# Performance work log

Hardware: AMD Instinct MI355X
Metric: run time of the kernel (lower is better)

Reference implementation:

```python
import jax, jax.numpy as jnp
import numpy as np

B, C, CI, H, W = 4, 128, 64, 96, 96  # batch, in_channels, inter_channels, spatial
SS = 2                                # sub_sample_factor (maxpool on phi and g)
BN_EPS = 1e-5


def conv1x1(x, w, b):
    # x: [B,C,H,W], w: [O,C], b: [O]
    return jnp.einsum('bchw,oc->bohw', x, w) + b[None, :, None, None]


def maxpool2(x):
    # 2x2 max pool, stride 2. x: [B,C,H,W]
    b, c, h, w = x.shape
    return x.reshape(b, c, h // 2, 2, w // 2, 2).max(axis=(3, 5))


def setup_inputs() -> dict:
    key = jax.random.key(0)
    ks = jax.random.split(key, 12)
    s_in = 1.0 / np.sqrt(C)
    s_ci = 1.0 / np.sqrt(CI)
    return {
        'x':        jax.random.normal(ks[0], (B, C, H, W), jnp.float32),
        'g_w':      jax.random.normal(ks[1], (CI, C), jnp.float32) * s_in,
        'g_b':      jax.random.normal(ks[2], (CI,), jnp.float32) * 0.01,
        'theta_w':  jax.random.normal(ks[3], (CI, C), jnp.float32) * s_in,
        'theta_b':  jax.random.normal(ks[4], (CI,), jnp.float32) * 0.01,
        'phi_w':    jax.random.normal(ks[5], (CI, C), jnp.float32) * s_in,
        'phi_b':    jax.random.normal(ks[6], (CI,), jnp.float32) * 0.01,
        'W_w':      jax.random.normal(ks[7], (C, CI), jnp.float32) * s_ci,
        'W_b':      jax.random.normal(ks[8], (C,), jnp.float32) * 0.01,
        'bn_gamma': jax.random.normal(ks[9], (C,), jnp.float32) * 0.1 + 1.0,
        'bn_beta':  jax.random.normal(ks[10], (C,), jnp.float32) * 0.1,
        'bn_mean':  jax.random.normal(ks[11], (C,), jnp.float32) * 0.1,
        'bn_var':   jax.random.uniform(jax.random.fold_in(key, 99), (C,), jnp.float32, 0.5, 1.5),
    }


def reference(x, g_w, g_b, theta_w, theta_b, phi_w, phi_b, W_w, W_b,
              bn_gamma, bn_beta, bn_mean, bn_var):
    b = x.shape[0]
    # g: conv1x1 -> maxpool(2) -> [B, N_kv, CI]
    g_x = maxpool2(conv1x1(x, g_w, g_b)).reshape(b, CI, -1).transpose(0, 2, 1)
    # theta: conv1x1 -> [B, N_q, CI]
    theta_x = conv1x1(x, theta_w, theta_b).reshape(b, CI, -1).transpose(0, 2, 1)
    # phi: conv1x1 -> maxpool(2) -> [B, CI, N_kv]
    phi_x = maxpool2(conv1x1(x, phi_w, phi_b)).reshape(b, CI, -1)
    # full affinity [B, N_q, N_kv], softmax over keys (embedded_gaussian)
    f = jnp.einsum('bqc,bck->bqk', theta_x, phi_x)
    attn = jax.nn.softmax(f, axis=-1)
    y = jnp.einsum('bqk,bkc->bqc', attn, g_x)            # [B, N_q, CI]
    y = y.transpose(0, 2, 1).reshape(b, CI, H, W)
    # W: conv1x1 (CI -> C) + BatchNorm (inference form) + residual
    W_y = conv1x1(y, W_w, W_b)
    inv = bn_gamma * jax.lax.rsqrt(bn_var + BN_EPS)
    W_y = W_y * inv[None, :, None, None] + (bn_beta - bn_mean * inv)[None, :, None, None]
    return W_y + x
```

## Files before the change

### kernel.cpp

```cpp
#include <hip/hip_runtime.h>
#include <hip/hip_bf16.h>

#define NB 4
#define NC 128
#define NH 96
#define NQ 9216
#define NKV 2304

typedef __bf16 bf8 __attribute__((ext_vector_type(8)));
typedef float f4 __attribute__((ext_vector_type(4)));
typedef unsigned short u16t;
typedef unsigned int u32t;
typedef u32t u32x4 __attribute__((ext_vector_type(4)));
typedef u16t u16x4v __attribute__((ext_vector_type(4)));

static __device__ __forceinline__ u16t f2bf(float f){
  u32t u = __builtin_bit_cast(u32t, f);
  u = (u + 0x7fffu + ((u >> 16) & 1u)) >> 16;
  return (u16t)u;
}
static __device__ __forceinline__ float bf2f(u16t h){
  return __builtin_bit_cast(float, ((u32t)h) << 16);
}

static __device__ __forceinline__ f4 mfma16(bf8 a, bf8 b, f4 c){
  return __builtin_amdgcn_mfma_f32_16x16x32_bf16(a, b, c, 0, 0, 0);
}

#define GLDS16(gp, lp) __builtin_amdgcn_global_load_lds( \
    (const u32t*)(gp), (u32t*)(lp), 16, 0, 0)

__global__ __launch_bounds__(256) void prep_weights(
    const float* __restrict__ g_w, const float* __restrict__ theta_w,
    const float* __restrict__ phi_w, const float* __restrict__ W_w,
    const float* __restrict__ W_b, const float* __restrict__ bn_gamma,
    const float* __restrict__ bn_beta, const float* __restrict__ bn_mean,
    const float* __restrict__ bn_var,
    u16t* __restrict__ wt_theta, u16t* __restrict__ wt_phi,
    u16t* __restrict__ wt_g, u16t* __restrict__ wt_W,
    float* __restrict__ alpha, float* __restrict__ beta2)
{
  int i = blockIdx.x * 256 + threadIdx.x;
  wt_theta[i] = f2bf(theta_w[i]);
  wt_phi[i]   = f2bf(phi_w[i]);
  wt_g[i]     = f2bf(g_w[i]);
  wt_W[i]     = f2bf(W_w[i]);
  if (blockIdx.x == 0 && threadIdx.x < 128){
    int t = threadIdx.x;
    float inv = bn_gamma[t] * rsqrtf(bn_var[t] + 1e-5f);
    alpha[t] = inv;
    beta2[t] = W_b[t]*inv + bn_beta[t] - bn_mean[t]*inv;
  }
}

__global__ __launch_bounds__(256) void conv3_pool(
    const float* __restrict__ x,
    const u16t* __restrict__ wt_theta, const u16t* __restrict__ wt_phi,
    const u16t* __restrict__ wt_g,
    const float* __restrict__ theta_b, const float* __restrict__ phi_b,
    const float* __restrict__ g_b,
    u16t* __restrict__ theta, u16t* __restrict__ phi, u16t* __restrict__ g_t)
{
  __shared__ __align__(16) u16t xt[64][136];
  const int blk = blockIdx.x;
  const int batch = blk / 144;
  const int t144 = blk % 144;
  const int ph = t144 / 3;
  const int pw0 = (t144 % 3) * 16;
  const int t = threadIdx.x;
  const float* xb = x + (size_t)batch * NC * NQ;

  #pragma unroll
  for (int i = 0; i < 8; ++i){
    int slot = i*256 + t;
    int c = slot >> 4;
    int quad = slot & 15;
    int row = quad >> 3, col4 = (quad & 7)*4;
    int q = (ph*2 + row)*NH + pw0*2 + col4;
    float4 v = *(const float4*)&xb[(size_t)c*NQ + q];
    int pl = row*32 + col4;
    xt[pl+0][c] = f2bf(v.x);
    xt[pl+1][c] = f2bf(v.y);
    xt[pl+2][c] = f2bf(v.z);
    xt[pl+3][c] = f2bf(v.w);
  }
  __syncthreads();

  const int w = t >> 6, l = t & 63, lm = l & 15, lg = l >> 4;
  auto PL = [](int pxi){
    return (((pxi>>1)&1) << 5) + 8*(pxi>>4) + 2*((pxi>>2)&3) + (pxi&1);
  };
  auto QROW = [&](int pxi){
    return (ph*2 + ((pxi>>1)&1))*NH + (pw0 + 4*(pxi>>4) + ((pxi>>2)&3))*2 + (pxi&1);
  };
  bf8 a[4];
  #pragma unroll
  for (int k = 0; k < 4; ++k)
    a[k] = *(const bf8*)&xt[PL(w*16 + lm)][k*32 + lg*8];

  const int kvbase = ph*48 + pw0;
  const int kv = kvbase + 4*w + lg;

  f4 Dth[4];
  #pragma unroll
  for (int s = 0; s < 4; ++s){
    float bv = theta_b[s*16 + lm];
    f4 D = {bv, bv, bv, bv};
    #pragma unroll
    for (int k = 0; k < 4; ++k){
      bf8 b = *(const bf8*)&wt_theta[(s*16 + lm)*128 + k*32 + lg*8];
      D = mfma16(a[k], b, D);
    }
    Dth[s] = D;
  }
  {
    u16t* pp = phi + (size_t)batch * NKV * 64;
    #pragma unroll
    for (int s = 0; s < 4; ++s){
      float bv = phi_b[s*16 + lm];
      f4 D = {bv, bv, bv, bv};
      #pragma unroll
      for (int k = 0; k < 4; ++k){
        bf8 b = *(const bf8*)&wt_phi[(s*16 + lm)*128 + k*32 + lg*8];
        D = mfma16(a[k], b, D);
      }
      float mx = fmaxf(fmaxf(D[0], D[1]), fmaxf(D[2], D[3]));
      pp[(size_t)kv*64 + s*16 + lm] = f2bf(mx);
    }
  }
  float gmx[4];
  #pragma unroll
  for (int s = 0; s < 4; ++s){
    float bv = g_b[s*16 + lm];
    f4 D = {bv, bv, bv, bv};
    #pragma unroll
    for (int k = 0; k < 4; ++k){
      bf8 b = *(const bf8*)&wt_g[(s*16 + lm)*128 + k*32 + lg*8];
      D = mfma16(a[k], b, D);
    }
    gmx[s] = fmaxf(fmaxf(D[0], D[1]), fmaxf(D[2], D[3]));
  }

  __syncthreads();
  u16t* tl = &xt[0][0];
  u16t* gl = &xt[0][0] + 4608;
  #pragma unroll
  for (int s = 0; s < 4; ++s){
    #pragma unroll
    for (int r = 0; r < 4; ++r)
      tl[(w*16 + lg*4 + r)*72 + s*16 + lm] = f2bf(Dth[s][r]);
    gl[(s*16 + lm)*20 + 4*w + lg] = f2bf(gmx[s]);
  }
  __syncthreads();
  {
    u16t* th = theta + (size_t)batch * NQ * 64;
    #pragma unroll
    for (int p = 0; p < 2; ++p){
      int slot = t + 256*p;
      int row = slot >> 3, piece = slot & 7;
      int q = QROW(row);
      *(bf8*)&th[(size_t)q*64 + piece*8] = *(const bf8*)&tl[row*72 + piece*8];
    }
  }
  {
    u16t* gt = g_t + (size_t)batch * 64 * NKV;
    int c = t >> 2, L = t & 3;
    int T = (kvbase >> 4) & 3;
    int kvg = kvbase & ~63;
    u16x4v v;
    #pragma unroll
    for (int u = 0; u < 4; ++u) v[u] = gl[c*20 + L*4 + u];
    *(u16x4v*)&gt[(size_t)c*NKV + kvg + (T>>1)*32 + ((T&1)<<2) + L*8] = v;
  }
}

#define G_OFF   32768

__global__ __launch_bounds__(384) void attn_partial(
    const u16t* __restrict__ theta, const u16t* __restrict__ phi,
    const u16t* __restrict__ g_t,
    u16t* __restrict__ yp_ws, float* __restrict__ sums_ws)
{
  __shared__ __align__(16) char SM[65536];

  const int bid = blockIdx.x;
  const int blkL = (bid & 7)*64 + (bid >> 3);
  const int batch = blkL >> 7;
  const int rem = blkL & 127;
  const int qb = (rem >> 1) * 144;
  const int khb = rem & 1;
  const int t = threadIdx.x;
  const int w = t >> 6, l = t & 63, lm = l & 15, lg = l >> 4;
  const int qw = w >> 1, khw = w & 1;

  const u16t* th = theta + ((size_t)batch*NQ + qb)*64;
  bf8 a[3][2];
  #pragma unroll
  for (int mr = 0; mr < 3; ++mr){
    a[mr][0] = *(const bf8*)&th[(qw*48 + mr*16 + lm)*64 + lg*8];
    a[mr][1] = *(const bf8*)&th[(qw*48 + mr*16 + lm)*64 + 32 + lg*8];
  }
  asm volatile("s_waitcnt vmcnt(0)" ::: "memory");

  const char* phc = (const char*)(phi + (size_t)batch*NKV*64);
  const char* gtc = (const char*)(g_t + (size_t)batch*64*NKV);

  auto STAGE = [&](int kt_s, int bufc){
    #pragma unroll
    for (int j = 0; j < 6; ++j){
      int u = w*6 + j;
      int ur = (u < 32) ? u : (u - 32);
      int khu = ur >> 4, isg = (ur >> 3) & 1, sub = ur & 7;
      int row = sub*8 + (l >> 3);
      int swz = ((l & 7) ^ (l >> 3)) << 4;
      int kb = khb*1152 + khu*576 + kt_s*64;
      char* dst = SM + (isg ? G_OFF : 0) + (khu*2 + bufc)*8192
                + sub*1024 + l*16;
      const char* src = isg
        ? gtc + (size_t)row*(NKV*2) + (size_t)kb*2 + swz
        : phc + (size_t)(kb + row)*128 + swz;
      GLDS16(src, dst);
    }
  };

  f4 Y[3][4];
  #pragma unroll
  for (int mr = 0; mr < 3; ++mr)
    #pragma unroll
    for (int s = 0; s < 4; ++s)
      Y[mr][s] = f4{0.f, 0.f, 0.f, 0.f};
  float lsum[3] = {0.f, 0.f, 0.f};

  STAGE(0, 0);

  for (int kt = 0; kt < 9; ++kt){
    const int buf = kt & 1;
    __builtin_amdgcn_s_barrier();
    asm volatile("" ::: "memory");
    if (kt < 8){
      STAGE(kt + 1, buf ^ 1);
      asm volatile("s_waitcnt vmcnt(6)" ::: "memory");
    } else {
      asm volatile("s_waitcnt vmcnt(0)" ::: "memory");
    }
    __builtin_amdgcn_s_barrier();
    asm volatile("" ::: "memory");
    __builtin_amdgcn_sched_barrier(0);

    const char* pb = SM + (khw*2 + buf)*8192;
    const char* gb = SM + G_OFF + (khw*2 + buf)*8192;
    const int m7 = lm & 7;

    bf8 bp[4][2];
    #pragma unroll
    for (int tt = 0; tt < 4; ++tt){
      int rb = (tt*16 + lm)*128;
      bp[tt][0] = *(const bf8*)(pb + rb + ((lg ^ m7) << 4));
      bp[tt][1] = *(const bf8*)(pb + rb + (((4 + lg) ^ m7) << 4));
    }
    bf8 bg[4][2];
    #pragma unroll
    for (int s = 0; s < 4; ++s){
      int rb = (s*16 + lm)*128;
      bg[s][0] = *(const bf8*)(gb + rb + ((lg ^ m7) << 4));
      bg[s][1] = *(const bf8*)(gb + rb + (((4 + lg) ^ m7) << 4));
    }

    #pragma unroll
    for (int mr = 0; mr < 3; ++mr){
      f4 S[4];
      #pragma unroll
      for (int tt = 0; tt < 4; ++tt){
        f4 z = {0.f, 0.f, 0.f, 0.f};
        z = mfma16(bp[tt][0], a[mr][0], z);
        S[tt] = mfma16(bp[tt][1], a[mr][1], z);
      }
      u32t wq[8];
      #pragma unroll
      for (int tt = 0; tt < 4; ++tt){
        float p0, p1, p2, p3;
        float a0 = fmaf(S[tt][0], 1.44269504f, -43.2808512f);
        float a1 = fmaf(S[tt][1], 1.44269504f, -43.2808512f);
        float a2 = fmaf(S[tt][2], 1.44269504f, -43.2808512f);
        float a3 = fmaf(S[tt][3], 1.44269504f, -43.2808512f);
        asm("v_exp_f32 %0, %1" : "=v"(p0) : "v"(a0));
        asm("v_exp_f32 %0, %1" : "=v"(p1) : "v"(a1));
        asm("v_exp_f32 %0, %1" : "=v"(p2) : "v"(a2));
        asm("v_exp_f32 %0, %1" : "=v"(p3) : "v"(a3));
        lsum[mr] += (p0 + p1) + (p2 + p3);
        asm("v_cvt_pk_bf16_f32 %0, %1, %2" : "=v"(wq[tt*2])   : "v"(p0), "v"(p1));
        asm("v_cvt_pk_bf16_f32 %0, %1, %2" : "=v"(wq[tt*2+1]) : "v"(p2), "v"(p3));
      }
      bf8 pa0 = __builtin_bit_cast(bf8, u32x4{wq[0], wq[1], wq[2], wq[3]});
      bf8 pa1 = __builtin_bit_cast(bf8, u32x4{wq[4], wq[5], wq[6], wq[7]});
      #pragma unroll
      for (int s = 0; s < 4; ++s){
        Y[mr][s] = mfma16(pa0, bg[s][0], Y[mr][s]);
        Y[mr][s] = mfma16(pa1, bg[s][1], Y[mr][s]);
      }
    }
  }

  float sv[3];
  #pragma unroll
  for (int mr = 0; mr < 3; ++mr){
    float s0 = lsum[mr];
    s0 += __shfl_xor(s0, 16);
    s0 += __shfl_xor(s0, 32);
    sv[mr] = s0;
  }

  __syncthreads();
  float (*ypL)[68] = (float (*)[68])SM;
  if (khw == 0){
    #pragma unroll
    for (int mr = 0; mr < 3; ++mr){
      #pragma unroll
      for (int s = 0; s < 4; ++s)
        #pragma unroll
        for (int r = 0; r < 4; ++r)
          ypL[qw*48 + mr*16 + lg*4 + r][s*16 + lm] = Y[mr][s][r];
      if (lg == 0)
        ypL[qw*48 + mr*16 + lm][64] = sv[mr];
    }
  }
  __syncthreads();
  if (khw == 1){
    #pragma unroll
    for (int mr = 0; mr < 3; ++mr){
      #pragma unroll
      for (int s = 0; s < 4; ++s)
        #pragma unroll
        for (int r = 0; r < 4; ++r)
          ypL[qw*48 + mr*16 + lg*4 + r][s*16 + lm] += Y[mr][s][r];
      if (lg == 0)
        ypL[qw*48 + mr*16 + lm][64] += sv[mr];
    }
  }
  __syncthreads();

  u16t* ypg = yp_ws + (size_t)blkL * (144*64);
  float* sg  = sums_ws + (size_t)blkL * 144;
  #pragma unroll
  for (int i = 0; i < 6; ++i){
    int idx = t + 384*i;
    int q = idx >> 4, c4 = (idx & 15)*4;
    u16x4v v;
    #pragma unroll
    for (int j = 0; j < 4; ++j) v[j] = f2bf(ypL[q][c4 + j]);
    *(u16x4v*)&ypg[q*64 + c4] = v;
  }
  if (t < 144) sg[t] = ypL[t][64];
}

__global__ __launch_bounds__(384) void combine_out(
    const u16t* __restrict__ yp_ws, const float* __restrict__ sums_ws,
    const u16t* __restrict__ wt_W,
    const float* __restrict__ alpha, const float* __restrict__ beta2,
    const float* __restrict__ x, float* __restrict__ out)
{
  __shared__ __align__(16) u16t yl[144][72];
  __shared__ __align__(16) float ol[144][131];
  const int bid = blockIdx.x;
  const int blk = (bid & 7)*32 + (bid >> 3);
  const int batch = blk >> 6;
  const int qb = (blk & 63) * 144;
  const int t = threadIdx.x;
  const int w = t >> 6, l = t & 63, lm = l & 15, lg = l >> 4;

  const u16t* pA = yp_ws + (size_t)(2*blk) * (144*64);
  const u16t* pB = pA + 144*64;
  const float* sA = sums_ws + (size_t)(2*blk) * 144;
  const float* sB = sA + 144;

  #pragma unroll
  for (int i = 0; i < 6; ++i){
    int idx = t + 384*i;
    int q = idx >> 4, c4 = (idx & 15)*4;
    float inv = 1.0f / (sA[q] + sB[q]);
    u16x4v a4 = *(const u16x4v*)&pA[q*64 + c4];
    u16x4v b4 = *(const u16x4v*)&pB[q*64 + c4];
    u16x4v v;
    #pragma unroll
    for (int j = 0; j < 4; ++j)
      v[j] = f2bf((bf2f(a4[j]) + bf2f(b4[j])) * inv);
    *(u16x4v*)&yl[q][c4] = v;
  }
  __syncthreads();

  #pragma unroll
  for (int i = 0; i < 12; ++i){
    int tau = w + 6*i;
    int qt = tau >> 3, ct = tau & 7;
    bf8 ya0 = *(const bf8*)&yl[qt*16 + lm][lg*8];
    bf8 ya1 = *(const bf8*)&yl[qt*16 + lm][32 + lg*8];
    const u16t* wr = wt_W + (ct*16 + lm)*64;
    bf8 b0 = *(const bf8*)&wr[lg*8];
    bf8 b1 = *(const bf8*)&wr[lg*8 + 32];
    f4 z = {0.f, 0.f, 0.f, 0.f};
    z = mfma16(ya0, b0, z);
    z = mfma16(ya1, b1, z);
    #pragma unroll
    for (int r = 0; r < 4; ++r)
      ol[qt*16 + lg*4 + r][ct*16 + lm] = z[r];
  }
  __syncthreads();

  const float* xb = x + (size_t)batch*NC*NQ + qb;
  float* ob = out + (size_t)batch*NC*NQ + qb;
  #pragma unroll
  for (int i = 0; i < 12; ++i){
    int idx = t + 384*i;
    int c = idx / 36, qv = idx % 36;
    float4 xv = *(const float4*)&xb[(size_t)c*NQ + qv*4];
    float al = alpha[c], be = beta2[c];
    float4 ov;
    ov.x = ol[qv*4 + 0][c]*al + be + xv.x;
    ov.y = ol[qv*4 + 1][c]*al + be + xv.y;
    ov.z = ol[qv*4 + 2][c]*al + be + xv.z;
    ov.w = ol[qv*4 + 3][c]*al + be + xv.w;
    *(float4*)&ob[(size_t)c*NQ + qv*4] = ov;
  }
}

extern "C" void kernel_launch(void* const* d_in, const int* in_sizes, int n_in,
                              void* d_out, int out_size, void* d_ws, size_t ws_size,
                              hipStream_t stream)
{
  const float* x       = (const float*)d_in[0];
  const float* g_w     = (const float*)d_in[1];
  const float* g_b     = (const float*)d_in[2];
  const float* theta_w = (const float*)d_in[3];
  const float* theta_b = (const float*)d_in[4];
  const float* phi_w   = (const float*)d_in[5];
  const float* phi_b   = (const float*)d_in[6];
  const float* W_w     = (const float*)d_in[7];
  const float* W_b     = (const float*)d_in[8];
  const float* bn_g    = (const float*)d_in[9];
  const float* bn_b    = (const float*)d_in[10];
  const float* bn_m    = (const float*)d_in[11];
  const float* bn_v    = (const float*)d_in[12];
  float* out = (float*)d_out;

  char* ws = (char*)d_ws;
  size_t off = 0;
  u16t* theta = (u16t*)(ws + off); off += (size_t)NB*NQ*64*2;
  u16t* phi   = (u16t*)(ws + off); off += (size_t)NB*NKV*64*2;
  u16t* g_t   = (u16t*)(ws + off); off += (size_t)NB*64*NKV*2;
  u16t* wt_theta = (u16t*)(ws + off); off += 64*128*2;
  u16t* wt_phi   = (u16t*)(ws + off); off += 64*128*2;
  u16t* wt_g     = (u16t*)(ws + off); off += 64*128*2;
  u16t* wt_W     = (u16t*)(ws + off); off += 128*64*2;
  float* alpha = (float*)(ws + off); off += 128*4;
  float* beta2 = (float*)(ws + off); off += 128*4;
  u16t* yp_ws  = (u16t*)(ws + off); off += (size_t)512*144*64*2;
  float* sums_ws = (float*)(ws + off); off += (size_t)512*144*4;
  if (off > ws_size) return;

  prep_weights<<<32, 256, 0, stream>>>(g_w, theta_w, phi_w, W_w, W_b,
                                       bn_g, bn_b, bn_m, bn_v,
                                       wt_theta, wt_phi, wt_g, wt_W, alpha, beta2);
  conv3_pool<<<576, 256, 0, stream>>>(x, wt_theta, wt_phi, wt_g,
                                      theta_b, phi_b, g_b, theta, phi, g_t);
  attn_partial<<<512, 384, 0, stream>>>(theta, phi, g_t, yp_ws, sums_ws);
  combine_out<<<256, 384, 0, stream>>>(yp_ws, sums_ws, wt_W, alpha, beta2, x, out);
}
```

Measured before the change: 81.18 us.

## Shrink attention tiles to 96 queries and 32-key stages for more blocks

Attention blocks drop from 144 to 96 query rows with 256 threads. The KV stage shrinks from 64 to 32 keys, so shared memory halves to 32KB and the K-loop runs 18 iterations instead of 9. Grid sizes for attention and combine grow to 768 and 384 blocks, which should improve occupancy and load balance across CUs. This costs more barriers and per-stage overhead, and the diff also swaps the conv prep's scalar bf16 conversion for packed cvt instructions.

```diff
diff --git a/kernel.cpp b/kernel.cpp
--- a/kernel.cpp
+++ b/kernel.cpp
@@ -79,10 +79,13 @@
     int q = (ph*2 + row)*NH + pw0*2 + col4;
     float4 v = *(const float4*)&xb[(size_t)c*NQ + q];
     int pl = row*32 + col4;
-    xt[pl+0][c] = f2bf(v.x);
-    xt[pl+1][c] = f2bf(v.y);
-    xt[pl+2][c] = f2bf(v.z);
-    xt[pl+3][c] = f2bf(v.w);
+    u32t lo, hi;
+    asm("v_cvt_pk_bf16_f32 %0, %1, %2" : "=v"(lo) : "v"(v.x), "v"(v.y));
+    asm("v_cvt_pk_bf16_f32 %0, %1, %2" : "=v"(hi) : "v"(v.z), "v"(v.w));
+    xt[pl+0][c] = (u16t)lo;
+    xt[pl+1][c] = (u16t)(lo >> 16);
+    xt[pl+2][c] = (u16t)hi;
+    xt[pl+3][c] = (u16t)(hi >> 16);
   }
   __syncthreads();
 
@@ -174,20 +177,19 @@
   }
 }
 
-#define G_OFF   32768
-
-__global__ __launch_bounds__(384) void attn_partial(
+
+__global__ __launch_bounds__(256) void attn_partial(
     const u16t* __restrict__ theta, const u16t* __restrict__ phi,
     const u16t* __restrict__ g_t,
     u16t* __restrict__ yp_ws, float* __restrict__ sums_ws)
 {
-  __shared__ __align__(16) char SM[65536];
+  __shared__ __align__(16) char SM[32768];
 
   const int bid = blockIdx.x;
-  const int blkL = (bid & 7)*64 + (bid >> 3);
-  const int batch = blkL >> 7;
-  const int rem = blkL & 127;
-  const int qb = (rem >> 1) * 144;
+  const int blkL = (bid & 7)*96 + (bid >> 3);
+  const int batch = blkL / 192;
+  const int rem = blkL % 192;
+  const int qb = (rem >> 1) * 96;
   const int khb = rem & 1;
   const int t = threadIdx.x;
   const int w = t >> 6, l = t & 63, lm = l & 15, lg = l >> 4;
@@ -207,18 +209,23 @@
 
   auto STAGE = [&](int kt_s, int bufc){
     #pragma unroll
-    for (int j = 0; j < 6; ++j){
-      int u = w*6 + j;
-      int ur = (u < 32) ? u : (u - 32);
-      int khu = ur >> 4, isg = (ur >> 3) & 1, sub = ur & 7;
-      int row = sub*8 + (l >> 3);
-      int swz = ((l & 7) ^ (l >> 3)) << 4;
-      int kb = khb*1152 + khu*576 + kt_s*64;
-      char* dst = SM + (isg ? G_OFF : 0) + (khu*2 + bufc)*8192
-                + sub*1024 + l*16;
-      const char* src = isg
-        ? gtc + (size_t)row*(NKV*2) + (size_t)kb*2 + swz
-        : phc + (size_t)(kb + row)*128 + swz;
+    for (int j = 0; j < 4; ++j){
+      int u = w*4 + j;
+      int khu = u >> 3, isg = (u >> 2) & 1, sub = u & 3;
+      int kb = khb*1152 + khu*576 + kt_s*32;
+      char* dst;
+      const char* src;
+      if (!isg){
+        int row = sub*8 + (l >> 3);
+        int swz = ((l & 7) ^ (l >> 3)) << 4;
+        dst = SM + (khu*2 + bufc)*4096 + sub*1024 + l*16;
+        src = phc + (size_t)(kb + row)*128 + swz;
+      } else {
+        int row = sub*16 + (l >> 2);
+        int swz = (((l & 3) ^ ((l >> 2) & 3)) << 4);
+        dst = SM + 16384 + (khu*2 + bufc)*4096 + sub*1024 + l*16;
+        src = gtc + (size_t)row*(NKV*2) + (size_t)kb*2 + swz;
+      }
       GLDS16(src, dst);
     }
   };
@@ -233,13 +240,13 @@
 
   STAGE(0, 0);
 
-  for (int kt = 0; kt < 9; ++kt){
+  for (int kt = 0; kt < 18; ++kt){
     const int buf = kt & 1;
     __builtin_amdgcn_s_barrier();
     asm volatile("" ::: "memory");
-    if (kt < 8){
+    if (kt < 17){
       STAGE(kt + 1, buf ^ 1);
-      asm volatile("s_waitcnt vmcnt(6)" ::: "memory");
+      asm volatile("s_waitcnt vmcnt(4)" ::: "memory");
     } else {
       asm volatile("s_waitcnt vmcnt(0)" ::: "memory");
     }
@@ -247,37 +254,36 @@
     asm volatile("" ::: "memory");
     __builtin_amdgcn_sched_barrier(0);
 
-    const char* pb = SM + (khw*2 + buf)*8192;
-    const char* gb = SM + G_OFF + (khw*2 + buf)*8192;
+    const char* pb = SM + (khw*2 + buf)*4096;
+    const char* gb = SM + 16384 + (khw*2 + buf)*4096;
     const int m7 = lm & 7;
 
-    bf8 bp[4][2];
-    #pragma unroll
-    for (int tt = 0; tt < 4; ++tt){
+    bf8 bp[2][2];
+    #pragma unroll
+    for (int tt = 0; tt < 2; ++tt){
       int rb = (tt*16 + lm)*128;
       bp[tt][0] = *(const bf8*)(pb + rb + ((lg ^ m7) << 4));
       bp[tt][1] = *(const bf8*)(pb + rb + (((4 + lg) ^ m7) << 4));
     }
-    bf8 bg[4][2];
+    bf8 bg[4];
     #pragma unroll
     for (int s = 0; s < 4; ++s){
-      int rb = (s*16 + lm)*128;
-      bg[s][0] = *(const bf8*)(gb + rb + ((lg ^ m7) << 4));
-      bg[s][1] = *(const bf8*)(gb + rb + (((4 + lg) ^ m7) << 4));
+      int rb = (s*16 + lm)*64;
+      bg[s] = *(const bf8*)(gb + rb + ((lg ^ (lm & 3)) << 4));
     }
 
     #pragma unroll
     for (int mr = 0; mr < 3; ++mr){
-      f4 S[4];
-      #pragma unroll
-      for (int tt = 0; tt < 4; ++tt){
+      f4 S[2];
+      #pragma unroll
+      for (int tt = 0; tt < 2; ++tt){
         f4 z = {0.f, 0.f, 0.f, 0.f};
         z = mfma16(bp[tt][0], a[mr][0], z);
         S[tt] = mfma16(bp[tt][1], a[mr][1], z);
       }
-      u32t wq[8];
-      #pragma unroll
-      for (int tt = 0; tt < 4; ++tt){
+      u32t wq[4];
+      #pragma unroll
+      for (int tt = 0; tt < 2; ++tt){
         float p0, p1, p2, p3;
         float a0 = fmaf(S[tt][0], 1.44269504f, -43.2808512f);
         float a1 = fmaf(S[tt][1], 1.44269504f, -43.2808512f);
@@ -291,13 +297,10 @@
         asm("v_cvt_pk_bf16_f32 %0, %1, %2" : "=v"(wq[tt*2])   : "v"(p0), "v"(p1));
         asm("v_cvt_pk_bf16_f32 %0, %1, %2" : "=v"(wq[tt*2+1]) : "v"(p2), "v"(p3));
       }
-      bf8 pa0 = __builtin_bit_cast(bf8, u32x4{wq[0], wq[1], wq[2], wq[3]});
-      bf8 pa1 = __builtin_bit_cast(bf8, u32x4{wq[4], wq[5], wq[6], wq[7]});
-      #pragma unroll
-      for (int s = 0; s < 4; ++s){
-        Y[mr][s] = mfma16(pa0, bg[s][0], Y[mr][s]);
-        Y[mr][s] = mfma16(pa1, bg[s][1], Y[mr][s]);
-      }
+      bf8 pa = __builtin_bit_cast(bf8, u32x4{wq[0], wq[1], wq[2], wq[3]});
+      #pragma unroll
+      for (int s = 0; s < 4; ++s)
+        Y[mr][s] = mfma16(pa, bg[s], Y[mr][s]);
     }
   }
 
@@ -339,43 +342,44 @@
   }
   __syncthreads();
 
-  u16t* ypg = yp_ws + (size_t)blkL * (144*64);
-  float* sg  = sums_ws + (size_t)blkL * 144;
+  u16t* ypg = yp_ws + (size_t)blkL * (96*64);
+  float* sg  = sums_ws + (size_t)blkL * 96;
   #pragma unroll
   for (int i = 0; i < 6; ++i){
-    int idx = t + 384*i;
+    int idx = t + 256*i;
     int q = idx >> 4, c4 = (idx & 15)*4;
     u16x4v v;
     #pragma unroll
     for (int j = 0; j < 4; ++j) v[j] = f2bf(ypL[q][c4 + j]);
     *(u16x4v*)&ypg[q*64 + c4] = v;
   }
-  if (t < 144) sg[t] = ypL[t][64];
-}
-
-__global__ __launch_bounds__(384) void combine_out(
+  if (t < 96) sg[t] = ypL[t][64];
+}
+
+__global__ __launch_bounds__(256) void combine_out(
     const u16t* __restrict__ yp_ws, const float* __restrict__ sums_ws,
     const u16t* __restrict__ wt_W,
     const float* __restrict__ alpha, const float* __restrict__ beta2,
     const float* __restrict__ x, float* __restrict__ out)
 {
-  __shared__ __align__(16) u16t yl[144][72];
-  __shared__ __align__(16) float ol[144][131];
+  __shared__ __align__(16) u16t yl[96][72];
+  __shared__ __align__(16) float ol[96][131];
   const int bid = blockIdx.x;
-  const int blk = (bid & 7)*32 + (bid >> 3);
-  const int batch = blk >> 6;
-  const int qb = (blk & 63) * 144;
+  const int blk = (bid & 7)*48 + (bid >> 3);
+  const int batch = blk / 96;
+  const int qg = blk % 96;
+  const int qb = qg * 96;
   const int t = threadIdx.x;
   const int w = t >> 6, l = t & 63, lm = l & 15, lg = l >> 4;
 
-  const u16t* pA = yp_ws + (size_t)(2*blk) * (144*64);
-  const u16t* pB = pA + 144*64;
-  const float* sA = sums_ws + (size_t)(2*blk) * 144;
-  const float* sB = sA + 144;
+  const u16t* pA = yp_ws + ((size_t)batch*192 + qg*2) * (96*64);
+  const u16t* pB = pA + 96*64;
+  const float* sA = sums_ws + ((size_t)batch*192 + qg*2) * 96;
+  const float* sB = sA + 96;
 
   #pragma unroll
   for (int i = 0; i < 6; ++i){
-    int idx = t + 384*i;
+    int idx = t + 256*i;
     int q = idx >> 4, c4 = (idx & 15)*4;
     float inv = 1.0f / (sA[q] + sB[q]);
     u16x4v a4 = *(const u16x4v*)&pA[q*64 + c4];
@@ -390,7 +394,7 @@
 
   #pragma unroll
   for (int i = 0; i < 12; ++i){
-    int tau = w + 6*i;
+    int tau = w + 4*i;
     int qt = tau >> 3, ct = tau & 7;
     bf8 ya0 = *(const bf8*)&yl[qt*16 + lm][lg*8];
     bf8 ya1 = *(const bf8*)&yl[qt*16 + lm][32 + lg*8];
@@ -410,8 +414,8 @@
   float* ob = out + (size_t)batch*NC*NQ + qb;
   #pragma unroll
   for (int i = 0; i < 12; ++i){
-    int idx = t + 384*i;
-    int c = idx / 36, qv = idx % 36;
+    int idx = t + 256*i;
+    int c = idx / 24, qv = idx % 24;
     float4 xv = *(const float4*)&xb[(size_t)c*NQ + qv*4];
     float al = alpha[c], be = beta2[c];
     float4 ov;
@@ -453,8 +457,8 @@
   u16t* wt_W     = (u16t*)(ws + off); off += 128*64*2;
   float* alpha = (float*)(ws + off); off += 128*4;
   float* beta2 = (float*)(ws + off); off += 128*4;
-  u16t* yp_ws  = (u16t*)(ws + off); off += (size_t)512*144*64*2;
-  float* sums_ws = (float*)(ws + off); off += (size_t)512*144*4;
+  u16t* yp_ws  = (u16t*)(ws + off); off += (size_t)768*96*64*2;
+  float* sums_ws = (float*)(ws + off); off += (size_t)768*96*4;
   if (off > ws_size) return;
 
   prep_weights<<<32, 256, 0, stream>>>(g_w, theta_w, phi_w, W_w, W_b,
@@ -462,6 +466,6 @@
                                        wt_theta, wt_phi, wt_g, wt_W, alpha, beta2);
   conv3_pool<<<576, 256, 0, stream>>>(x, wt_theta, wt_phi, wt_g,
                                       theta_b, phi_b, g_b, theta, phi, g_t);
-  attn_partial<<<512, 384, 0, stream>>>(theta, phi, g_t, yp_ws, sums_ws);
-  combine_out<<<256, 384, 0, stream>>>(yp_ws, sums_ws, wt_W, alpha, beta2, x, out);
-}
+  attn_partial<<<768, 256, 0, stream>>>(theta, phi, g_t, yp_ws, sums_ws);
+  combine_out<<<384, 256, 0, stream>>>(yp_ws, sums_ws, wt_W, alpha, beta2, x, out);
+}
```

Measured after the change: 75.99 us. 6.4% less time.
